# Kernel tuning notes

Measured on AMD Instinct MI355X. Metric: run time of the kernel, lower is better.

## Reference

```python
import jax, jax.numpy as jnp
import numpy as np

BATCH = 8192
IN_F = 1024
OUT_F = 1024
GRID = 5
K = 3            # spline order (degree)
SCALE = 1.0      # scale_spline


def setup_inputs() -> dict:
    key = jax.random.key(0)
    k1, k2, k3 = jax.random.split(key, 3)
    x = jax.random.normal(k1, (BATCH, IN_F), dtype=jnp.float32)
    # kaiming_uniform_(a=sqrt(5)) on (out,in) -> U(-1/sqrt(in), 1/sqrt(in))
    bound = 1.0 / np.sqrt(IN_F)
    base_weight = jax.random.uniform(k2, (OUT_F, IN_F), jnp.float32, -bound, bound)
    # normal(mean=0, std=0.1), shape (out, in, grid_size + spline_order)
    spline_weight = 0.1 * jax.random.normal(k3, (OUT_F, IN_F, GRID + K), dtype=jnp.float32)
    # extended knot vector: uniform grid on [-1,1] with spacing h, padded by K knots each side
    h = 2.0 / GRID
    knots = jnp.arange(-K, GRID + K + 1, dtype=jnp.float32) * h - 1.0  # (GRID+2K+1,)
    grid = jnp.tile(knots[None, :], (IN_F, 1))                          # (in, GRID+2K+1)
    return {"x": x, "base_weight": base_weight, "spline_weight": spline_weight, "grid": grid}


def _b_splines(x, grid, k):
    # x: (B, in), grid: (in, G+2k+1) -> basis: (B, in, G+k)
    xe = x[..., None]  # (B, in, 1)
    basis = ((xe >= grid[:, :-1]) & (xe < grid[:, 1:])).astype(x.dtype)  # degree-0, (B,in,G+2k)
    for p in range(1, k + 1):  # Cox-de Boor recursion, degree p
        left = (xe - grid[:, :-(p + 1)]) / (grid[:, p:-1] - grid[:, :-(p + 1)]) * basis[..., :-1]
        right = (grid[:, (p + 1):] - xe) / (grid[:, (p + 1):] - grid[:, 1:-p]) * basis[..., 1:]
        basis = left + right
    return basis


def reference(x, base_weight, spline_weight, grid):
    base = x @ base_weight.T                                   # (B, out)
    basis = _b_splines(x, grid, K)                             # (B, in, G+K)
    spline = jnp.einsum('bic,oic->bo', basis, spline_weight)   # (B, out)
    return base + SCALE * spline
```

## Files before the change

### kernel.cpp

```cpp
#include <hip/hip_runtime.h>


#define BATCH 8192
#define IN_F  1024
#define OUT_F 1024
#define NC    9
#define KAUG  (IN_F * NC)

typedef float  f32x4  __attribute__((ext_vector_type(4)));
typedef __bf16 bf16x8 __attribute__((ext_vector_type(8)));
typedef unsigned short u16;
typedef u16 u16x8 __attribute__((ext_vector_type(8)));

__device__ __forceinline__ u16 f2bf(float f) {
  unsigned int u = __builtin_bit_cast(unsigned int, f);
  u += 0x7FFFu + ((u >> 16) & 1u);
  return (u16)(u >> 16);
}

__device__ __forceinline__ void bspline8(float x, float bas[8]) {
  const float t  = (x + 2.2f) * 2.5f;
  const float cf = floorf(t);
  const int   c  = (int)cf;
  const float u  = t - cf;
  const float u2 = u * u, u3 = u2 * u;
  const float um = 1.0f - u;
  const float b0 = um * um * um * (1.0f / 6.0f);
  const float b1 = (3.0f * u3 - 6.0f * u2 + 4.0f) * (1.0f / 6.0f);
  const float b2 = (-3.0f * u3 + 3.0f * u2 + 3.0f * u + 1.0f) * (1.0f / 6.0f);
  const float b3 = u3 * (1.0f / 6.0f);
#pragma unroll
  for (int j = 0; j < 8; ++j) {
    const int r = j - c + 3;
    bas[j] = (r == 0) ? b0 : (r == 1) ? b1 : (r == 2) ? b2 : (r == 3) ? b3 : 0.0f;
  }
}

__global__ __launch_bounds__(256) void build_AW(const float* __restrict__ X,
                                                const float* __restrict__ BW,
                                                const float* __restrict__ SW,
                                                u16* __restrict__ Aa,
                                                u16* __restrict__ Wa) {
  const int idx = blockIdx.x * 256 + threadIdx.x;
  if (idx < BATCH * 128) {
    const int b  = idx >> 7;
    const int i0 = (idx & 127) << 3;
    const float4* xp = (const float4*)(X + (size_t)b * IN_F + i0);
    float4 xa = xp[0], xb = xp[1];
    float xs[8] = {xa.x, xa.y, xa.z, xa.w, xb.x, xb.y, xb.z, xb.w};
    u16x8 out[9];
#pragma unroll
    for (int e = 0; e < 8; ++e) {
      const float x = xs[e];
      out[0][e] = f2bf(x);
      float bas[8];
      bspline8(x, bas);
#pragma unroll
      for (int c = 0; c < 8; ++c) out[c + 1][e] = f2bf(bas[c]);
    }
    u16* row = Aa + (size_t)b * KAUG + i0;
#pragma unroll
    for (int c = 0; c < 9; ++c) *(u16x8*)(row + c * IN_F) = out[c];
  } else {
    const int wdx = idx - BATCH * 128;
    const int o  = wdx >> 7;
    const int i0 = (wdx & 127) << 3;
    u16x8 out[9];
    const float4* bp = (const float4*)(BW + (size_t)o * IN_F + i0);
    float4 b0 = bp[0], b1 = bp[1];
    float bs[8] = {b0.x, b0.y, b0.z, b0.w, b1.x, b1.y, b1.z, b1.w};
#pragma unroll
    for (int e = 0; e < 8; ++e) out[0][e] = f2bf(bs[e]);
    const float4* sp = (const float4*)(SW + ((size_t)o * IN_F + i0) * 8);
#pragma unroll
    for (int e = 0; e < 8; ++e) {
      float4 s0 = sp[e * 2], s1 = sp[e * 2 + 1];
      out[1][e] = f2bf(s0.x);
      out[2][e] = f2bf(s0.y);
      out[3][e] = f2bf(s0.z);
      out[4][e] = f2bf(s0.w);
      out[5][e] = f2bf(s1.x);
      out[6][e] = f2bf(s1.y);
      out[7][e] = f2bf(s1.z);
      out[8][e] = f2bf(s1.w);
    }
    u16* row = Wa + (size_t)o * KAUG + i0;
#pragma unroll
    for (int c = 0; c < 9; ++c) *(u16x8*)(row + c * IN_F) = out[c];
  }
}

#define BM 256
#define BN 128
#define BK 64
#define NT (KAUG / BK)

__device__ __forceinline__ void async16(const u16* g, u16* l) {
  __builtin_amdgcn_global_load_lds(
      (const __attribute__((address_space(1))) u16*)g,
      (__attribute__((address_space(3))) u16*)l,
      16, 0, 0);
}

__global__ __launch_bounds__(512) void gemm_bt(
    const u16* __restrict__ A,
    const u16* __restrict__ B,
    float* __restrict__ C) {
  constexpr int N = OUT_F, K = KAUG;
  __shared__ __align__(16) u16 sm[3][24576];

  const int tid = threadIdx.x;

  const int bid = blockIdx.x;
  const int wg  = (bid & 7) * 32 + (bid >> 3);
  const int bm  = wg >> 3;
  const int bn  = wg & 7;

  const int lane = tid & 63;
  const int wid  = tid >> 6;
  const int wm   = wid >> 1;
  const int wn   = wid & 1;
  const int fr   = lane & 15;
  const int hi   = lane >> 4;

  const int ak0 = ((hi      ^ (fr & 7)) << 3);
  const int ak1 = (((4 | hi) ^ (fr & 7)) << 3);
  int arow[4], brow[4];
#pragma unroll
  for (int m = 0; m < 4; ++m) arow[m] = (wm * 64 + m * 16 + fr) * 64;
#pragma unroll
  for (int n = 0; n < 4; ++n) brow[n] = 16384 + (wn * 64 + n * 16 + fr) * 64;

  const int trow = tid >> 3;
  const int gsrc = (tid & 7) ^ (trow & 7);
  const u16* Asrc = A + (size_t)(bm * BM + trow) * K + gsrc * 8;
  const u16* Bsrc = B + (size_t)(bn * BN + trow) * K + gsrc * 8;

#pragma unroll
  for (int tt = 0; tt < 2; ++tt) {
    u16* dA = &sm[tt][0] + tid * 8;
    u16* dB = &sm[tt][16384] + tid * 8;
    const size_t kg = (size_t)tt * BK;
    async16(Asrc + kg, dA);
    async16(Asrc + (size_t)64  * K + kg, dA + 4096);
    async16(Asrc + (size_t)128 * K + kg, dA + 8192);
    async16(Asrc + (size_t)192 * K + kg, dA + 12288);
    async16(Bsrc + kg, dB);
    async16(Bsrc + (size_t)64  * K + kg, dB + 4096);
  }

  f32x4 acc[4][4] = {};

  for (int t = 0; t < NT; ++t) {
    const int cur = t % 3;
    const int nxt = (t + 2) % 3;
    const bool pf = (t + 2) < NT;
    const size_t kg = (size_t)(t + 2) * BK;
    const u16* s0 = &sm[cur][0];
    u16* dA = &sm[nxt][0] + tid * 8;
    u16* dB = &sm[nxt][16384] + tid * 8;

    if (t < NT - 1) asm volatile("s_waitcnt vmcnt(6)" ::: "memory");
    else            asm volatile("s_waitcnt vmcnt(0)" ::: "memory");
    __builtin_amdgcn_s_barrier();
    __builtin_amdgcn_sched_barrier(0);

    bf16x8 aa[4], bf[4];
#pragma unroll
    for (int n = 0; n < 4; ++n) bf[n] = *(const bf16x8*)(s0 + brow[n] + ak0);
#pragma unroll
    for (int m = 0; m < 4; ++m) aa[m] = *(const bf16x8*)(s0 + arow[m] + ak0);
    if (pf) {
      async16(Asrc + kg, dA);
      async16(Asrc + (size_t)64  * K + kg, dA + 4096);
      async16(Asrc + (size_t)128 * K + kg, dA + 8192);
    }
    __builtin_amdgcn_s_setprio(1);
#pragma unroll
    for (int m = 0; m < 4; ++m)
#pragma unroll
      for (int n = 0; n < 4; ++n)
        acc[m][n] = __builtin_amdgcn_mfma_f32_16x16x32_bf16(aa[m], bf[n], acc[m][n], 0, 0, 0);
    __builtin_amdgcn_s_setprio(0);
#pragma unroll
    for (int n = 0; n < 4; ++n) bf[n] = *(const bf16x8*)(s0 + brow[n] + ak1);
#pragma unroll
    for (int m = 0; m < 4; ++m) aa[m] = *(const bf16x8*)(s0 + arow[m] + ak1);
    if (pf) {
      async16(Asrc + (size_t)192 * K + kg, dA + 12288);
      async16(Bsrc + kg, dB);
      async16(Bsrc + (size_t)64  * K + kg, dB + 4096);
    }
    __builtin_amdgcn_s_setprio(1);
#pragma unroll
    for (int m = 0; m < 4; ++m)
#pragma unroll
      for (int n = 0; n < 4; ++n)
        acc[m][n] = __builtin_amdgcn_mfma_f32_16x16x32_bf16(aa[m], bf[n], acc[m][n], 0, 0, 0);
    __builtin_amdgcn_s_setprio(0);
  }

  const int r0 = bm * BM + wm * 64 + hi * 4;
  const int c0 = bn * BN + wn * 64 + fr;
#pragma unroll
  for (int i = 0; i < 4; ++i)
#pragma unroll
    for (int j = 0; j < 4; ++j) {
      float* cp = C + (size_t)(r0 + i * 16) * N + (c0 + j * 16);
#pragma unroll
      for (int r = 0; r < 4; ++r) cp[(size_t)r * N] = acc[i][j][r];
    }
}

extern "C" void kernel_launch(void* const* d_in, const int* in_sizes, int n_in,
                              void* d_out, int out_size, void* d_ws, size_t ws_size,
                              hipStream_t stream) {
  const float* x  = (const float*)d_in[0];
  const float* bw = (const float*)d_in[1];
  const float* sw = (const float*)d_in[2];
  float* out = (float*)d_out;

  u16* Aaug = (u16*)d_ws;
  u16* Waug = Aaug + (size_t)BATCH * KAUG;

  build_AW<<<dim3((BATCH + OUT_F) * 128 / 256), 256, 0, stream>>>(x, bw, sw, Aaug, Waug);
  gemm_bt<<<dim3(BATCH / BM * (OUT_F / BN)), 512, 0, stream>>>(Aaug, Waug, out);
}
```

Measured before the change: 273.1 us.

## Fuse basis/weight build and GEMM into one persistent kernel with grid barrier

Merges the augmented-operand build kernel and the bf16 MFMA GEMM into a single 256-block kernel. Each block first builds its share of the A and W operands, then all blocks meet at a grid-wide barrier built on an atomic counter before the GEMM phase starts. The counter lives in the first bytes of the output buffer and is zeroed by a memset beforehand. This removes one kernel boundary and its launch and drain gap, but it adds a memset, a spin barrier that assumes all 256 blocks are co-resident, and a possible race when GEMM results later overwrite the counter.

```diff
diff --git a/kernel.cpp b/kernel.cpp
--- a/kernel.cpp
+++ b/kernel.cpp
@@ -36,15 +36,37 @@
   }
 }
 
-__global__ __launch_bounds__(256) void build_AW(const float* __restrict__ X,
-                                                const float* __restrict__ BW,
-                                                const float* __restrict__ SW,
-                                                u16* __restrict__ Aa,
-                                                u16* __restrict__ Wa) {
-  const int idx = blockIdx.x * 256 + threadIdx.x;
-  if (idx < BATCH * 128) {
-    const int b  = idx >> 7;
-    const int i0 = (idx & 127) << 3;
+#define BM 256
+#define BN 128
+#define BK 64
+#define NT (KAUG / BK)
+
+__device__ __forceinline__ void async16(const u16* g, u16* l) {
+  __builtin_amdgcn_global_load_lds(
+      (const __attribute__((address_space(1))) u16*)g,
+      (__attribute__((address_space(3))) u16*)l,
+      16, 0, 0);
+}
+
+__global__ __launch_bounds__(512) void kan_fused(
+    const float* __restrict__ X,
+    const float* __restrict__ BW,
+    const float* __restrict__ SW,
+    u16* __restrict__ Aa,
+    u16* __restrict__ Wa,
+    float* __restrict__ C,
+    unsigned int* __restrict__ ctr) {
+  constexpr int N = OUT_F, K = KAUG;
+  __shared__ __align__(16) u16 sm[3][24576];
+
+  const int tid = threadIdx.x;
+  const int gid = blockIdx.x * 512 + tid;
+
+#pragma unroll 4
+  for (int u = 0; u < 8; ++u) {
+    const int unit = gid + u * 131072;
+    const int b  = unit >> 7;
+    const int i0 = (unit & 127) << 3;
     const float4* xp = (const float4*)(X + (size_t)b * IN_F + i0);
     float4 xa = xp[0], xb = xp[1];
     float xs[8] = {xa.x, xa.y, xa.z, xa.w, xb.x, xb.y, xb.z, xb.w};
@@ -61,10 +83,10 @@
     u16* row = Aa + (size_t)b * KAUG + i0;
 #pragma unroll
     for (int c = 0; c < 9; ++c) *(u16x8*)(row + c * IN_F) = out[c];
-  } else {
-    const int wdx = idx - BATCH * 128;
-    const int o  = wdx >> 7;
-    const int i0 = (wdx & 127) << 3;
+  }
+  {
+    const int o  = gid >> 7;
+    const int i0 = (gid & 127) << 3;
     u16x8 out[9];
     const float4* bp = (const float4*)(BW + (size_t)o * IN_F + i0);
     float4 b0 = bp[0], b1 = bp[1];
@@ -88,28 +110,18 @@
 #pragma unroll
     for (int c = 0; c < 9; ++c) *(u16x8*)(row + c * IN_F) = out[c];
   }
-}
-
-#define BM 256
-#define BN 128
-#define BK 64
-#define NT (KAUG / BK)
-
-__device__ __forceinline__ void async16(const u16* g, u16* l) {
-  __builtin_amdgcn_global_load_lds(
-      (const __attribute__((address_space(1))) u16*)g,
-      (__attribute__((address_space(3))) u16*)l,
-      16, 0, 0);
-}
-
-__global__ __launch_bounds__(512) void gemm_bt(
-    const u16* __restrict__ A,
-    const u16* __restrict__ B,
-    float* __restrict__ C) {
-  constexpr int N = OUT_F, K = KAUG;
-  __shared__ __align__(16) u16 sm[3][24576];
-
-  const int tid = threadIdx.x;
+
+  __threadfence();
+  __syncthreads();
+  if (tid == 0) {
+    __hip_atomic_fetch_add(ctr, 1u, __ATOMIC_ACQ_REL, __HIP_MEMORY_SCOPE_AGENT);
+    unsigned int v;
+    do {
+      v = __hip_atomic_load(ctr, __ATOMIC_ACQUIRE, __HIP_MEMORY_SCOPE_AGENT);
+      if (v < 256u) __builtin_amdgcn_s_sleep(8);
+    } while (v < 256u);
+  }
+  __syncthreads();
 
   const int bid = blockIdx.x;
   const int wg  = (bid & 7) * 32 + (bid >> 3);
@@ -133,8 +145,8 @@
 
   const int trow = tid >> 3;
   const int gsrc = (tid & 7) ^ (trow & 7);
-  const u16* Asrc = A + (size_t)(bm * BM + trow) * K + gsrc * 8;
-  const u16* Bsrc = B + (size_t)(bn * BN + trow) * K + gsrc * 8;
+  const u16* Asrc = Aa + (size_t)(bm * BM + trow) * K + gsrc * 8;
+  const u16* Bsrc = Wa + (size_t)(bn * BN + trow) * K + gsrc * 8;
 
 #pragma unroll
   for (int tt = 0; tt < 2; ++tt) {
@@ -223,6 +235,7 @@
   u16* Aaug = (u16*)d_ws;
   u16* Waug = Aaug + (size_t)BATCH * KAUG;
 
-  build_AW<<<dim3((BATCH + OUT_F) * 128 / 256), 256, 0, stream>>>(x, bw, sw, Aaug, Waug);
-  gemm_bt<<<dim3(BATCH / BM * (OUT_F / BN)), 512, 0, stream>>>(Aaug, Waug, out);
-}
+  hipMemsetAsync(d_out, 0, 8, stream);
+  kan_fused<<<dim3(256), 512, 0, stream>>>(x, bw, sw, Aaug, Waug, out,
+                                           (unsigned int*)d_out);
+}
```

Result: slower. 421.5 us (+54.4%).
